# Kernel tuning notes

Measured on AMD Instinct MI355X. Metric: run time of the kernel, lower is better.

Reference implementation:

```python
import jax, jax.numpy as jnp
import numpy as np

TEMPERATURE = 0.07
NORM_EPS = 1e-12  # matches torch F.normalize eps


def setup_inputs() -> dict:
    key = jax.random.key(0)
    k1, k2 = jax.random.split(key)
    emb = jax.random.normal(k1, (4, 256, 61, 61), dtype=jnp.float32)
    targets = jax.random.randint(k2, (4, 61, 61), 0, 5, dtype=jnp.int64)
    return {"emb": emb, "targets": targets}


def reference(emb, targets):
    n, c, h, w = emb.shape
    # (N,C,H,W) -> (N*H*W, C), L2-normalized per pixel
    feats = emb.transpose(0, 2, 3, 1).reshape(-1, c)
    norms = jnp.maximum(jnp.linalg.norm(feats, axis=1, keepdims=True), NORM_EPS)
    feats = feats / norms
    labels = targets.reshape(-1)  # (T,)
    T = labels.shape[0]

    sim = jnp.matmul(feats, feats.T) / TEMPERATURE  # (T,T)
    exp_sim = jnp.exp(sim)

    eye = jnp.eye(T, dtype=bool)
    pos_mask = (labels[None, :] == labels[:, None]) & ~eye  # (T,T) bool

    sum_pos = jnp.sum(jnp.where(pos_mask, exp_sim, 0.0), axis=1)  # (T,)
    sum_all = exp_sim.sum(axis=1) - jnp.exp(jnp.diagonal(sim))    # (T,)

    valid = sum_pos > 0
    # safe log: substitute 1.0 where invalid to avoid -inf/NaN, then mask
    safe_pos = jnp.where(valid, sum_pos, 1.0)
    safe_all = jnp.where(valid, sum_all, 1.0)
    per_row = jnp.where(valid, -(jnp.log(safe_pos) - jnp.log(safe_all)), 0.0)
    loss = per_row.sum() / jnp.maximum(valid.sum(), 1).astype(per_row.dtype)
    return loss
```

## Files before the change

### kernel.cpp

```cpp
#include <hip/hip_runtime.h>
#include <cstdint>
#include <cstddef>

#define T_REAL 14884
#define TPAD   15360
#define CDIM   256
#define HW     3721
#define NRB    60
#define NSL    16
#define TPS    15
#define NT     240
#define NPADJ  476.0f

static constexpr float SQRT_SCALE = 4.53981598f;

typedef _Float16 f16x8  __attribute__((ext_vector_type(8)));
typedef float    f32x16 __attribute__((ext_vector_type(16)));

__device__ __forceinline__ float exp2_fast(float x) {
#if __has_builtin(__builtin_amdgcn_exp2f)
    return __builtin_amdgcn_exp2f(x);
#else
    return exp2f(x);
#endif
}

#define OFF_FEATS 0u
#define SZ_FEATS  ((unsigned)TPAD * CDIM * 2u)
#define OFF_LAB   (OFF_FEATS + SZ_FEATS)
#define OFF_RANK  (OFF_LAB + (unsigned)TPAD * 4u)
#define OFF_TCL   (OFF_RANK + 59648u)
#define OFF_DONE  (OFF_TCL + 1024u)
#define OFF_PART  (OFF_DONE + 128u)
#define SZ_PART   ((unsigned)NRB * NSL * 256u * 8u)
#define OFF_ACC   (OFF_PART + SZ_PART)

__global__ void k_sort(const int* __restrict__ targets, int* __restrict__ rank,
                       int* __restrict__ labels, int* __restrict__ tcl,
                       float* __restrict__ accum, int* __restrict__ done) {
    __shared__ int h[5], cur[5], soffs[6];
    const int tid = threadIdx.x, lane = tid & 63;
    if (tid < 5) h[tid] = 0;
    if (tid == 8) { accum[0] = 0.f; accum[1] = 0.f; }
    if (tid == 9) done[0] = 0;
    __syncthreads();

    for (int t = tid; t < T_REAL; t += 1024) {
        const int c = targets[t];
#pragma unroll
        for (int cl = 0; cl < 5; ++cl) {
            unsigned long long m = __ballot(c == cl);
            if (c == cl && lane == __ffsll(m) - 1) atomicAdd(&h[cl], (int)__popcll(m));
        }
    }
    __syncthreads();
    if (tid == 0) {
        int o = 0;
#pragma unroll
        for (int c = 0; c < 5; ++c) { soffs[c] = o; cur[c] = o; o += h[c]; }
        soffs[5] = o;
    }
    __syncthreads();

    for (int t = tid; t < T_REAL; t += 1024) {
        const int c = targets[t];
#pragma unroll
        for (int cl = 0; cl < 5; ++cl) {
            unsigned long long m = __ballot(c == cl);
            if (c == cl) {
                const int leader = __ffsll(m) - 1;
                int base = 0;
                if (lane == leader) base = atomicAdd(&cur[cl], (int)__popcll(m));
                base = __shfl(base, leader);
                const int r = base + (int)__popcll(m & ((1ull << lane) - 1ull));
                rank[t] = r;
                labels[r] = c;
            }
        }
    }
    for (int t = T_REAL + tid; t < TPAD; t += 1024) labels[t] = -1;

    for (int t = tid; t < NT; t += 1024) {
        const int lo = t * 64, hi = lo + 64;
        int tc = -2;
        if (lo >= T_REAL) tc = -1;
        else {
#pragma unroll
            for (int c = 0; c < 5; ++c)
                if (lo >= soffs[c] && hi <= soffs[c + 1]) tc = c;
        }
        tcl[t] = tc;
    }
}

__global__ void k_prep(const float* __restrict__ emb, const int* __restrict__ rank,
                       _Float16* __restrict__ feats) {
    const int tid = threadIdx.x;
    const int bx = blockIdx.x, n = blockIdx.y;

    if (bx == 59) {
        const int r0 = T_REAL + n * 119;
        f16x8 z = {0, 0, 0, 0, 0, 0, 0, 0};
        for (int c = tid; c < 119 * 32; c += 256) {
            int rr = r0 + (c >> 5), cc = c & 31;
            *reinterpret_cast<f16x8*>(feats + (size_t)rr * CDIM + cc * 8) = z;
        }
        return;
    }

    __shared__ float tile[64][257];
    __shared__ float sspart[4][64];
    const int lane = tid & 63, w = tid >> 6;
    const int px0 = bx * 64;
    const int hw = px0 + lane;

    float ssq = 0.f;
    for (int ci = w; ci < CDIM; ci += 4) {
        float v = (hw < HW) ? emb[((size_t)(n * CDIM + ci)) * HW + hw] : 0.f;
        tile[lane][ci] = v;
        ssq += v * v;
    }
    sspart[w][lane] = ssq;
    __syncthreads();

    const int pp = tid >> 2, q = tid & 3;
    float s2 = sspart[q][pp];
    s2 += __shfl_xor(s2, 1);
    s2 += __shfl_xor(s2, 2);
    const float inv = SQRT_SCALE / fmaxf(sqrtf(s2), 1e-12f);

    const int hwp = px0 + pp;
    if (hwp < HW) {
        const int row = rank[n * HW + hwp];
        _Float16* dst = feats + (size_t)row * CDIM + q * 64;
#pragma unroll
        for (int g = 0; g < 8; ++g) {
            const int gg = g ^ q;
            f16x8 o;
#pragma unroll
            for (int e = 0; e < 8; ++e) o[e] = (_Float16)(tile[pp][q * 64 + gg * 8 + e] * inv);
            *reinterpret_cast<f16x8*>(dst + gg * 8) = o;
        }
    }
}

__device__ __forceinline__ void stage_half(const _Float16* __restrict__ feats, int jbase,
                                           _Float16* bufp, int tid, int half) {
#pragma unroll
    for (int s4 = 0; s4 < 4; ++s4) {
        const int sweep = half * 4 + s4;
        const int ch = sweep * 256 + tid;
        const int j  = ch >> 5;
        const int c  = ch & 31;
        const int swz = (j & 7) ^ (((j >> 3) & 3) << 1);
        const _Float16* src = feats + ((size_t)(jbase + j)) * CDIM + (c ^ swz) * 8;
        __builtin_amdgcn_global_load_lds(
            (const __attribute__((address_space(1))) void*)src,
            (__attribute__((address_space(3))) void*)(bufp + (size_t)ch * 8),
            16, 0, 0);
    }
}

__global__ __launch_bounds__(256, 2) void k_main(const _Float16* __restrict__ feats,
                                                 const int* __restrict__ labels,
                                                 const int* __restrict__ tcl,
                                                 float2* __restrict__ partials) {
    __shared__ __align__(16) _Float16 buf[2][64 * 256];
    const int tid  = threadIdx.x;
    const int w    = tid >> 6, lane = tid & 63;
    const int lo   = lane & 31, hi = lane >> 5;
    const int rb = blockIdx.x, slice = blockIdx.y;
    const int ibase = rb * 256 + w * 64;

    const int labi0 = labels[ibase + lo];
    const int labi1 = labels[ibase + 32 + lo];

    f16x8 b0[16], b1[16];
    {
        const f16x8* r0 = (const f16x8*)(feats + (size_t)(ibase + lo) * CDIM + hi * 8);
        const f16x8* r1 = (const f16x8*)(feats + (size_t)(ibase + 32 + lo) * CDIM + hi * 8);
#pragma unroll
        for (int ks = 0; ks < 16; ++ks) { b0[ks] = r0[ks * 2]; b1[ks] = r1[ks * 2]; }
    }

    const int s  = (lo & 7) ^ (((lo >> 3) & 3) << 1);
    const int sp = s >> 1;
    const int x0h = (s & 1) << 3;
    int idx4[4];
#pragma unroll
    for (int m = 0; m < 4; ++m)
        idx4[m] = lo * 256 + ((hi << 3) ^ x0h) + ((m ^ sp) << 4);

    float accA0 = 0.f, accP0 = 0.f, accA1 = 0.f, accP1 = 0.f;

    stage_half(feats, slice * 64, &buf[0][0], tid, 0);
    stage_half(feats, slice * 64, &buf[0][0], tid, 1);

#pragma unroll 1
    for (int ti = 0; ti < TPS; ++ti) {
        const int jt = slice + ti * NSL;
        const bool nxt = (ti + 1 < TPS);
        const int tc = tcl[__builtin_amdgcn_readfirstlane(jt)];

        if (nxt) {
            stage_half(feats, (jt + NSL) * 64, &buf[(ti + 1) & 1][0], tid, 0);
            asm volatile("s_waitcnt vmcnt(4)" ::: "memory");
        } else {
            asm volatile("s_waitcnt vmcnt(0)" ::: "memory");
        }
        __builtin_amdgcn_s_barrier();
        __builtin_amdgcn_sched_barrier(0);

        const _Float16* bc = &buf[ti & 1][0];
        f32x16 c00 = {0,0,0,0,0,0,0,0,0,0,0,0,0,0,0,0};
        f32x16 c01 = c00, c10 = c00, c11 = c00;

#pragma unroll
        for (int ph = 0; ph < 4; ++ph) {
            f16x8 a0[4], a1[4];
#pragma unroll
            for (int m = 0; m < 4; ++m) {
                const int off = idx4[m] + (ph << 6);
                a0[m] = *reinterpret_cast<const f16x8*>(bc + off);
                a1[m] = *reinterpret_cast<const f16x8*>(bc + 8192 + off);
            }
            if (ph == 0 && nxt)
                stage_half(feats, (jt + NSL) * 64, &buf[(ti + 1) & 1][0], tid, 1);
            asm volatile("s_waitcnt lgkmcnt(0)" ::: "memory");
            __builtin_amdgcn_sched_barrier(0);
            __builtin_amdgcn_s_setprio(1);
#pragma unroll
            for (int m = 0; m < 4; ++m) {
                const int ks = ph * 4 + m;
                c00 = __builtin_amdgcn_mfma_f32_32x32x16_f16(a0[m], b0[ks], c00, 0, 0, 0);
                c01 = __builtin_amdgcn_mfma_f32_32x32x16_f16(a0[m], b1[ks], c01, 0, 0, 0);
                c10 = __builtin_amdgcn_mfma_f32_32x32x16_f16(a1[m], b0[ks], c10, 0, 0, 0);
                c11 = __builtin_amdgcn_mfma_f32_32x32x16_f16(a1[m], b1[ks], c11, 0, 0, 0);
            }
            __builtin_amdgcn_s_setprio(0);
        }

        if (tc != -2) {
            float t0 = 0.f, t1 = 0.f, t2 = 0.f, t3 = 0.f;
#pragma unroll
            for (int v = 0; v < 16; ++v) {
                t0 += exp2_fast(c00[v]);
                t1 += exp2_fast(c01[v]);
                t2 += exp2_fast(c10[v]);
                t3 += exp2_fast(c11[v]);
            }
            accA0 += t0 + t2; accA1 += t1 + t3;
            accP0 += (tc == labi0) ? (t0 + t2) : 0.f;
            accP1 += (tc == labi1) ? (t1 + t3) : 0.f;
        } else {
            const int jb = jt * 64;
#pragma unroll
            for (int q = 0; q < 4; ++q) {
                const int4 lj0 = *reinterpret_cast<const int4*>(labels + jb + q * 8 + hi * 4);
                const int4 lj1 = *reinterpret_cast<const int4*>(labels + jb + 32 + q * 8 + hi * 4);
#pragma unroll
                for (int r = 0; r < 4; ++r) {
                    const int l0 = (r == 0) ? lj0.x : (r == 1) ? lj0.y : (r == 2) ? lj0.z : lj0.w;
                    const int l1 = (r == 0) ? lj1.x : (r == 1) ? lj1.y : (r == 2) ? lj1.z : lj1.w;
                    const int v = q * 4 + r;
                    float e;
                    e = exp2_fast(c00[v]); accA0 += e; accP0 += (l0 == labi0) ? e : 0.f;
                    e = exp2_fast(c01[v]); accA1 += e; accP1 += (l0 == labi1) ? e : 0.f;
                    e = exp2_fast(c10[v]); accA0 += e; accP0 += (l1 == labi0) ? e : 0.f;
                    e = exp2_fast(c11[v]); accA1 += e; accP1 += (l1 == labi1) ? e : 0.f;
                }
            }
        }
        __builtin_amdgcn_s_barrier();
    }

    float n0 = 0.f, n1 = 0.f;
#pragma unroll
    for (int ks = 0; ks < 16; ++ks)
#pragma unroll
        for (int e = 0; e < 8; ++e) {
            float v0 = (float)b0[ks][e]; n0 += v0 * v0;
            float v1 = (float)b1[ks][e]; n1 += v1 * v1;
        }
    n0 += __shfl_xor(n0, 32); n1 += __shfl_xor(n1, 32);

    accA0 += __shfl_xor(accA0, 32); accP0 += __shfl_xor(accP0, 32);
    accA1 += __shfl_xor(accA1, 32); accP1 += __shfl_xor(accP1, 32);

    if (((rb * 4 + w) & (NSL - 1)) == slice) {
        float e0 = exp2_fast(n0), e1 = exp2_fast(n1);
        accA0 -= e0; accP0 -= e0;
        accA1 -= e1; accP1 -= e1;
    }

    if (hi == 0) {
        size_t base = ((size_t)(rb * NSL + slice)) * 256 + w * 64;
        partials[base + lo]      = make_float2(accA0, accP0);
        partials[base + 32 + lo] = make_float2(accA1, accP1);
    }
}

__global__ void k_reduce(const float2* __restrict__ partials, float* __restrict__ accum,
                         int* __restrict__ done, float* __restrict__ out) {
    const int rb = blockIdx.x;
    const int rl = threadIdx.x;
    const int t  = rb * 256 + rl;
    float sA = -NPADJ, sP = 0.f;
#pragma unroll
    for (int s = 0; s < NSL; ++s) {
        float2 v = partials[((size_t)(rb * NSL + s)) * 256 + rl];
        sA += v.x; sP += v.y;
    }
    float per = 0.f, cnt = 0.f;
    if (t < T_REAL && sP > 0.f) {
        per = logf(sA) - logf(sP);
        cnt = 1.f;
    }
#pragma unroll
    for (int off = 32; off >= 1; off >>= 1) {
        per += __shfl_xor(per, off);
        cnt += __shfl_xor(cnt, off);
    }
    if ((rl & 63) == 0) { atomicAdd(&accum[0], per); atomicAdd(&accum[1], cnt); }
    __syncthreads();
    if (rl == 0) {
        __threadfence();
        if (atomicAdd(done, 1) == NRB - 1) {
            float a = atomicAdd(&accum[0], 0.f);
            float c = atomicAdd(&accum[1], 0.f);
            out[0] = a / fmaxf(c, 1.f);
        }
    }
}

extern "C" void kernel_launch(void* const* d_in, const int* in_sizes, int n_in,
                              void* d_out, int out_size, void* d_ws, size_t ws_size,
                              hipStream_t stream) {
    const float* emb     = (const float*)d_in[0];
    const int*   targets = (const int*)d_in[1];
    float*       out     = (float*)d_out;
    char*        ws      = (char*)d_ws;

    _Float16* feats    = (_Float16*)(ws + OFF_FEATS);
    int*      labels   = (int*)(ws + OFF_LAB);
    int*      rank     = (int*)(ws + OFF_RANK);
    int*      tcl      = (int*)(ws + OFF_TCL);
    int*      done     = (int*)(ws + OFF_DONE);
    float2*   partials = (float2*)(ws + OFF_PART);
    float*    accum    = (float*)(ws + OFF_ACC);

    k_sort  <<<dim3(1),        dim3(1024), 0, stream>>>(targets, rank, labels, tcl, accum, done);
    k_prep  <<<dim3(60, 4),    dim3(256),  0, stream>>>(emb, rank, feats);
    k_main  <<<dim3(NRB, NSL), dim3(256),  0, stream>>>(feats, labels, tcl, partials);
    k_reduce<<<dim3(NRB),      dim3(256),  0, stream>>>(partials, accum, done, out);
}
```

Baseline: 261.5 us.

## Use 512-thread blocks with one 32-row B fragment per wave in main kernel

```diff
diff --git a/kernel.cpp b/kernel.cpp
--- a/kernel.cpp
+++ b/kernel.cpp
@@ -144,12 +144,11 @@
     }
 }
 
-__device__ __forceinline__ void stage_half(const _Float16* __restrict__ feats, int jbase,
-                                           _Float16* bufp, int tid, int half) {
-#pragma unroll
-    for (int s4 = 0; s4 < 4; ++s4) {
-        const int sweep = half * 4 + s4;
-        const int ch = sweep * 256 + tid;
+__device__ __forceinline__ void stage_tile(const _Float16* __restrict__ feats, int jbase,
+                                           _Float16* bufp, int tid) {
+#pragma unroll
+    for (int sweep = 0; sweep < 4; ++sweep) {
+        const int ch = sweep * 512 + tid;
         const int j  = ch >> 5;
         const int c  = ch & 31;
         const int swz = (j & 7) ^ (((j >> 3) & 3) << 1);
@@ -161,7 +160,7 @@
     }
 }
 
-__global__ __launch_bounds__(256, 2) void k_main(const _Float16* __restrict__ feats,
+__global__ __launch_bounds__(512, 2) void k_main(const _Float16* __restrict__ feats,
                                                  const int* __restrict__ labels,
                                                  const int* __restrict__ tcl,
                                                  float2* __restrict__ partials) {
@@ -170,17 +169,15 @@
     const int w    = tid >> 6, lane = tid & 63;
     const int lo   = lane & 31, hi = lane >> 5;
     const int rb = blockIdx.x, slice = blockIdx.y;
-    const int ibase = rb * 256 + w * 64;
-
-    const int labi0 = labels[ibase + lo];
-    const int labi1 = labels[ibase + 32 + lo];
-
-    f16x8 b0[16], b1[16];
+    const int ibase = rb * 256 + w * 32;
+
+    const int labi = labels[ibase + lo];
+
+    f16x8 b[16];
     {
         const f16x8* r0 = (const f16x8*)(feats + (size_t)(ibase + lo) * CDIM + hi * 8);
-        const f16x8* r1 = (const f16x8*)(feats + (size_t)(ibase + 32 + lo) * CDIM + hi * 8);
-#pragma unroll
-        for (int ks = 0; ks < 16; ++ks) { b0[ks] = r0[ks * 2]; b1[ks] = r1[ks * 2]; }
+#pragma unroll
+        for (int ks = 0; ks < 16; ++ks) b[ks] = r0[ks * 2];
     }
 
     const int s  = (lo & 7) ^ (((lo >> 3) & 3) << 1);
@@ -191,19 +188,17 @@
     for (int m = 0; m < 4; ++m)
         idx4[m] = lo * 256 + ((hi << 3) ^ x0h) + ((m ^ sp) << 4);
 
-    float accA0 = 0.f, accP0 = 0.f, accA1 = 0.f, accP1 = 0.f;
-
-    stage_half(feats, slice * 64, &buf[0][0], tid, 0);
-    stage_half(feats, slice * 64, &buf[0][0], tid, 1);
+    float accA = 0.f, accP = 0.f;
+
+    stage_tile(feats, slice * 64, &buf[0][0], tid);
 
 #pragma unroll 1
     for (int ti = 0; ti < TPS; ++ti) {
         const int jt = slice + ti * NSL;
-        const bool nxt = (ti + 1 < TPS);
         const int tc = tcl[__builtin_amdgcn_readfirstlane(jt)];
 
-        if (nxt) {
-            stage_half(feats, (jt + NSL) * 64, &buf[(ti + 1) & 1][0], tid, 0);
+        if (ti + 1 < TPS) {
+            stage_tile(feats, (jt + NSL) * 64, &buf[(ti + 1) & 1][0], tid);
             asm volatile("s_waitcnt vmcnt(4)" ::: "memory");
         } else {
             asm volatile("s_waitcnt vmcnt(0)" ::: "memory");
@@ -212,46 +207,27 @@
         __builtin_amdgcn_sched_barrier(0);
 
         const _Float16* bc = &buf[ti & 1][0];
-        f32x16 c00 = {0,0,0,0,0,0,0,0,0,0,0,0,0,0,0,0};
-        f32x16 c01 = c00, c10 = c00, c11 = c00;
-
-#pragma unroll
-        for (int ph = 0; ph < 4; ++ph) {
-            f16x8 a0[4], a1[4];
-#pragma unroll
-            for (int m = 0; m < 4; ++m) {
-                const int off = idx4[m] + (ph << 6);
-                a0[m] = *reinterpret_cast<const f16x8*>(bc + off);
-                a1[m] = *reinterpret_cast<const f16x8*>(bc + 8192 + off);
+        f32x16 cA = {0,0,0,0,0,0,0,0,0,0,0,0,0,0,0,0};
+        f32x16 cB = cA;
+
+#pragma unroll
+        for (int ks = 0; ks < 16; ++ks) {
+            const int off = idx4[ks & 3] + ((ks & 12) << 4);
+            const f16x8 a_lo = *reinterpret_cast<const f16x8*>(bc + off);
+            const f16x8 a_hi = *reinterpret_cast<const f16x8*>(bc + 8192 + off);
+            cA = __builtin_amdgcn_mfma_f32_32x32x16_f16(a_lo, b[ks], cA, 0, 0, 0);
+            cB = __builtin_amdgcn_mfma_f32_32x32x16_f16(a_hi, b[ks], cB, 0, 0, 0);
+        }
+
+        if (tc != -2) {
+            float t0 = 0.f, t1 = 0.f;
+#pragma unroll
+            for (int v = 0; v < 16; ++v) {
+                t0 += exp2_fast(cA[v]);
+                t1 += exp2_fast(cB[v]);
             }
-            if (ph == 0 && nxt)
-                stage_half(feats, (jt + NSL) * 64, &buf[(ti + 1) & 1][0], tid, 1);
-            asm volatile("s_waitcnt lgkmcnt(0)" ::: "memory");
-            __builtin_amdgcn_sched_barrier(0);
-            __builtin_amdgcn_s_setprio(1);
-#pragma unroll
-            for (int m = 0; m < 4; ++m) {
-                const int ks = ph * 4 + m;
-                c00 = __builtin_amdgcn_mfma_f32_32x32x16_f16(a0[m], b0[ks], c00, 0, 0, 0);
-                c01 = __builtin_amdgcn_mfma_f32_32x32x16_f16(a0[m], b1[ks], c01, 0, 0, 0);
-                c10 = __builtin_amdgcn_mfma_f32_32x32x16_f16(a1[m], b0[ks], c10, 0, 0, 0);
-                c11 = __builtin_amdgcn_mfma_f32_32x32x16_f16(a1[m], b1[ks], c11, 0, 0, 0);
-            }
-            __builtin_amdgcn_s_setprio(0);
-        }
-
-        if (tc != -2) {
-            float t0 = 0.f, t1 = 0.f, t2 = 0.f, t3 = 0.f;
-#pragma unroll
-            for (int v = 0; v < 16; ++v) {
-                t0 += exp2_fast(c00[v]);
-                t1 += exp2_fast(c01[v]);
-                t2 += exp2_fast(c10[v]);
-                t3 += exp2_fast(c11[v]);
-            }
-            accA0 += t0 + t2; accA1 += t1 + t3;
-            accP0 += (tc == labi0) ? (t0 + t2) : 0.f;
-            accP1 += (tc == labi1) ? (t1 + t3) : 0.f;
+            accA += t0 + t1;
+            accP += (tc == labi) ? (t0 + t1) : 0.f;
         } else {
             const int jb = jt * 64;
 #pragma unroll
@@ -264,39 +240,31 @@
                     const int l1 = (r == 0) ? lj1.x : (r == 1) ? lj1.y : (r == 2) ? lj1.z : lj1.w;
                     const int v = q * 4 + r;
                     float e;
-                    e = exp2_fast(c00[v]); accA0 += e; accP0 += (l0 == labi0) ? e : 0.f;
-                    e = exp2_fast(c01[v]); accA1 += e; accP1 += (l0 == labi1) ? e : 0.f;
-                    e = exp2_fast(c10[v]); accA0 += e; accP0 += (l1 == labi0) ? e : 0.f;
-                    e = exp2_fast(c11[v]); accA1 += e; accP1 += (l1 == labi1) ? e : 0.f;
+                    e = exp2_fast(cA[v]); accA += e; accP += (l0 == labi) ? e : 0.f;
+                    e = exp2_fast(cB[v]); accA += e; accP += (l1 == labi) ? e : 0.f;
                 }
             }
         }
         __builtin_amdgcn_s_barrier();
     }
 
-    float n0 = 0.f, n1 = 0.f;
+    float nsq = 0.f;
 #pragma unroll
     for (int ks = 0; ks < 16; ++ks)
 #pragma unroll
-        for (int e = 0; e < 8; ++e) {
-            float v0 = (float)b0[ks][e]; n0 += v0 * v0;
-            float v1 = (float)b1[ks][e]; n1 += v1 * v1;
-        }
-    n0 += __shfl_xor(n0, 32); n1 += __shfl_xor(n1, 32);
-
-    accA0 += __shfl_xor(accA0, 32); accP0 += __shfl_xor(accP0, 32);
-    accA1 += __shfl_xor(accA1, 32); accP1 += __shfl_xor(accP1, 32);
-
-    if (((rb * 4 + w) & (NSL - 1)) == slice) {
-        float e0 = exp2_fast(n0), e1 = exp2_fast(n1);
-        accA0 -= e0; accP0 -= e0;
-        accA1 -= e1; accP1 -= e1;
+        for (int e = 0; e < 8; ++e) { float v0 = (float)b[ks][e]; nsq += v0 * v0; }
+    nsq += __shfl_xor(nsq, 32);
+
+    accA += __shfl_xor(accA, 32);
+    accP += __shfl_xor(accP, 32);
+
+    if (((rb * 4 + (w >> 1)) & (NSL - 1)) == slice) {
+        float e0 = exp2_fast(nsq);
+        accA -= e0; accP -= e0;
     }
 
     if (hi == 0) {
-        size_t base = ((size_t)(rb * NSL + slice)) * 256 + w * 64;
-        partials[base + lo]      = make_float2(accA0, accP0);
-        partials[base + 32 + lo] = make_float2(accA1, accP1);
+        partials[((size_t)(rb * NSL + slice)) * 256 + w * 32 + lo] = make_float2(accA, accP);
     }
 }
 
@@ -351,6 +319,6 @@
 
     k_sort  <<<dim3(1),        dim3(1024), 0, stream>>>(targets, rank, labels, tcl, accum, done);
     k_prep  <<<dim3(60, 4),    dim3(256),  0, stream>>>(emb, rank, feats);
-    k_main  <<<dim3(NRB, NSL), dim3(256),  0, stream>>>(feats, labels, tcl, partials);
+    k_main  <<<dim3(NRB, NSL), dim3(512),  0, stream>>>(feats, labels, tcl, partials);
     k_reduce<<<dim3(NRB),      dim3(256),  0, stream>>>(partials, accum, done, out);
 }
```

Result: faster. 252.2 us (-3.5%).
